# Performance work log

Measured on AMD Instinct MI355X. Metric: run time of the kernel, lower is better.

The kernel has to match this reference:

```python
import jax, jax.numpy as jnp
import numpy as np

SIZE = 2.0            # scene extent, matches init size
N_LEVELS = 16         # Instant-NGP default
TABLE_SIZE = 1 << 19  # hash entries per level (power of 2)
FEAT = 2              # embedding_length per level
BASE_RES = 16         # init resolution
MAX_RES = 2048
N_POINTS = 1 << 21

_OFFS = np.array([[(c >> d) & 1 for d in range(3)] for c in range(8)])  # [8,3] corner bits
_PRIMES = np.array([1, 2654435761, 805459861], dtype=np.uint32)         # NGP spatial hash primes


def setup_inputs() -> dict:
    key = jax.random.key(0)
    k1, k2 = jax.random.split(key)
    xyz = (jax.random.uniform(k1, (N_POINTS, 3), dtype=jnp.float32) - 0.5) * SIZE
    tables = jax.random.normal(k2, (N_LEVELS, TABLE_SIZE, FEAT), dtype=jnp.float32) * 1e-2
    # geometric resolution schedule 16 -> 2048 over 16 levels
    growth = (MAX_RES / BASE_RES) ** (np.arange(N_LEVELS) / (N_LEVELS - 1))
    resolutions = jnp.asarray(np.floor(BASE_RES * growth).astype(np.int32))
    return {"xyz": xyz, "tables": tables, "resolutions": resolutions}


def _encode(xyz, tables, resolutions):
    u = xyz / SIZE + 0.5                              # [N,3] in [0,1)
    offs_u = jnp.asarray(_OFFS.astype(np.uint32))     # [8,3]
    offs_f = jnp.asarray(_OFFS.astype(np.float32))    # [8,3]
    primes = jnp.asarray(_PRIMES)

    def level(_, xs):
        table, res = xs                               # [T,F], scalar int32
        p = u * res.astype(jnp.float32)               # [N,3]
        p0 = jnp.floor(p)
        w = p - p0                                    # trilinear fractions [N,3]
        c = p0.astype(jnp.uint32)[:, None, :] + offs_u[None]     # [N,8,3]
        h = (c[..., 0] * primes[0]) ^ (c[..., 1] * primes[1]) ^ (c[..., 2] * primes[2])
        idx = (h & jnp.uint32(TABLE_SIZE - 1)).astype(jnp.int32)  # [N,8]
        feats = table[idx]                                        # [N,8,F] gather
        wc = jnp.prod(jnp.where(offs_f[None] > 0, w[:, None, :], 1.0 - w[:, None, :]), axis=-1)  # [N,8]
        return None, jnp.sum(feats * wc[..., None], axis=1)      # [N,F]

    _, embs = jax.lax.scan(level, None, (tables, resolutions))   # [L,N,F]
    n = xyz.shape[0]
    return jnp.transpose(embs, (1, 0, 2)).reshape(n, N_LEVELS * FEAT)


def reference(xyz, tables, resolutions):
    return _encode(xyz, tables, resolutions)
```

## Files before the change

kernel.cpp:

```cpp
#include <hip/hip_runtime.h>
#include <hip/hip_fp16.h>

#define NLV 16
#define TBL (1u << 19)
#define TMASK (TBL - 1u)
#define P1 2654435761u
#define P2 805459861u
#define NBIN (1 << 15)

typedef float vf2 __attribute__((ext_vector_type(2)));
typedef float vf4 __attribute__((ext_vector_type(4)));
typedef unsigned vu2 __attribute__((ext_vector_type(2)));
typedef unsigned vu4 __attribute__((ext_vector_type(4)));
typedef int vi4 __attribute__((ext_vector_type(4)));

__device__ __forceinline__ vf2 h2_to_f2(unsigned bits) {
    union { unsigned u; __half2 h; } c; c.u = bits;
    float2 f = __half22float2(c.h);
    vf2 r; r.x = f.x; r.y = f.y; return r;
}
__device__ __forceinline__ unsigned f2_to_h2(float a, float b) {
    union { __half2 h; unsigned u; } c; c.h = __floats2half2_rn(a, b);
    return c.u;
}

__device__ __forceinline__ unsigned mort5(unsigned v) {
    v &= 31u;
    v = (v | (v << 16)) & 0x030000FFu;
    v = (v | (v << 8))  & 0x0300F00Fu;
    v = (v | (v << 4))  & 0x030C30C3u;
    v = (v | (v << 2))  & 0x09249249u;
    return v;
}

__device__ __forceinline__ unsigned bin_of(float ux, float uy, float uz) {
    unsigned bx = min(31u, (unsigned)(ux * 32.0f));
    unsigned by = min(31u, (unsigned)(uy * 32.0f));
    unsigned bz = min(31u, (unsigned)(uz * 32.0f));
    return mort5(bx) | (mort5(by) << 1) | (mort5(bz) << 2);
}

__global__ __launch_bounds__(256) void convert_tables(
    const float* __restrict__ tables, unsigned* __restrict__ htab, int total)
{
    int i = blockIdx.x * 256 + threadIdx.x;
    int e0 = i * 2;
    if (e0 >= total) return;
    vf4 v = *(const vf4*)(tables + (size_t)e0 * 2);
    vu2 o; o.x = f2_to_h2(v.x, v.y); o.y = f2_to_h2(v.z, v.w);
    *(vu2*)(htab + e0) = o;
}

__global__ __launch_bounds__(256) void hist_kernel(
    const float* __restrict__ xyz, unsigned* __restrict__ hist, int n)
{
    int p = blockIdx.x * 256 + threadIdx.x;
    if (p >= n) return;
    float ux = xyz[(size_t)p * 3 + 0] * 0.5f + 0.5f;
    float uy = xyz[(size_t)p * 3 + 1] * 0.5f + 0.5f;
    float uz = xyz[(size_t)p * 3 + 2] * 0.5f + 0.5f;
    atomicAdd(&hist[bin_of(ux, uy, uz)], 1u);
}

__global__ __launch_bounds__(1024) void scan_bins(unsigned* __restrict__ hist)
{
    __shared__ unsigned part[1024];
    int t = threadIdx.x;
    int base = t * (NBIN / 1024);
    unsigned s = 0;
    for (int j = 0; j < NBIN / 1024; ++j) s += hist[base + j];
    part[t] = s;
    __syncthreads();
    for (int off = 1; off < 1024; off <<= 1) {
        unsigned v = (t >= off) ? part[t - off] : 0u;
        __syncthreads();
        part[t] += v;
        __syncthreads();
    }
    unsigned run = (t == 0) ? 0u : part[t - 1];
    for (int j = 0; j < NBIN / 1024; ++j) {
        unsigned tmp = hist[base + j];
        hist[base + j] = run;
        run += tmp;
    }
}

__global__ __launch_bounds__(256) void scatter_kernel(
    const float* __restrict__ xyz, unsigned* __restrict__ start,
    vf4* __restrict__ u4s, int* __restrict__ orig, int n)
{
    int p = blockIdx.x * 256 + threadIdx.x;
    if (p >= n) return;
    float ux = xyz[(size_t)p * 3 + 0] * 0.5f + 0.5f;
    float uy = xyz[(size_t)p * 3 + 1] * 0.5f + 0.5f;
    float uz = xyz[(size_t)p * 3 + 2] * 0.5f + 0.5f;
    unsigned pos = atomicAdd(&start[bin_of(ux, uy, uz)], 1u);
    orig[pos] = p;
    vf4 r; r.x = ux; r.y = uy; r.z = uz; r.w = 0.0f;
    u4s[pos] = r;
}

__global__ __launch_bounds__(256) void ngp_gather_s(
    const vf4* __restrict__ u4s,
    const unsigned* __restrict__ htab,
    const int* __restrict__ resolutions,
    unsigned* __restrict__ wsout,
    int n, int nbPerLevel)
{
    int L = blockIdx.x / nbPerLevel;
    int chunk = blockIdx.x % nbPerLevel;
    int p0 = chunk * 1024 + (int)threadIdx.x;

    float res = (float)resolutions[L];
    const unsigned* __restrict__ tab = htab + (size_t)L * TBL;
    unsigned* __restrict__ wl = wsout + (size_t)L * n;

    unsigned idx[4][8];
    float wx[4], wyz[4][4];
    bool valid[4];

#pragma unroll
    for (int q = 0; q < 4; ++q) {
        int p = p0 + q * 256;
        valid[q] = (p < n);
        int pp = valid[q] ? p : 0;
        vf4 u = u4s[pp];
        float px = u.x * res, py = u.y * res, pz = u.z * res;
        float fx = floorf(px), fy = floorf(py), fz = floorf(pz);
        float wxl = px - fx, wyl = py - fy, wzl = pz - fz;
        unsigned cx = (unsigned)fx, cy = (unsigned)fy, cz = (unsigned)fz;
        unsigned hx0 = cx, hx1 = cx + 1u;
        unsigned hy0 = cy * P1, hy1 = hy0 + P1;
        unsigned hz0 = cz * P2, hz1 = hz0 + P2;
#pragma unroll
        for (int c = 0; c < 8; ++c)
            idx[q][c] = ((((c & 1) ? hx1 : hx0) ^
                          ((c & 2) ? hy1 : hy0) ^
                          ((c & 4) ? hz1 : hz0)) & TMASK);
        float vy = 1.0f - wyl, vz = 1.0f - wzl;
        wx[q] = wxl;
        wyz[q][0] = vy * vz;  wyz[q][1] = wyl * vz;
        wyz[q][2] = vy * wzl; wyz[q][3] = wyl * wzl;
    }

    unsigned d[4][8];
#pragma unroll
    for (int q = 0; q < 4; ++q)
#pragma unroll
        for (int c = 0; c < 8; ++c)
            d[q][c] = tab[idx[q][c]];

#pragma unroll
    for (int q = 0; q < 4; ++q) {
        float vx = 1.0f - wx[q];
        float a0 = 0.0f, a1 = 0.0f;
#pragma unroll
        for (int c = 0; c < 8; ++c) {
            float w = wyz[q][c >> 1] * ((c & 1) ? wx[q] : vx);
            vf2 f = h2_to_f2(d[q][c]);
            a0 += f.x * w;
            a1 += f.y * w;
        }
        int p = p0 + q * 256;
        if (valid[q]) wl[p] = f2_to_h2(a0, a1);
    }
}

__global__ __launch_bounds__(256) void ngp_finalize_s(
    const unsigned* __restrict__ ws, const int* __restrict__ orig,
    float* __restrict__ out, int n)
{
    int t = blockIdx.x * 256 + threadIdx.x;
    int i = t * 4;
    if (i >= n) return;

    if (i + 3 < n && (n & 3) == 0) {
        vu4 m[NLV];
#pragma unroll
        for (int L = 0; L < NLV; ++L)
            m[L] = *(const vu4*)(ws + (size_t)L * n + i);
        vi4 og = *(const vi4*)(orig + i);
#pragma unroll
        for (int pt = 0; pt < 4; ++pt) {
            int op = pt == 0 ? og.x : pt == 1 ? og.y : pt == 2 ? og.z : og.w;
            vf4* o = (vf4*)(out + (size_t)op * (NLV * 2));
#pragma unroll
            for (int j = 0; j < 8; ++j) {
                unsigned ba = pt == 0 ? m[2 * j].x : pt == 1 ? m[2 * j].y
                             : pt == 2 ? m[2 * j].z : m[2 * j].w;
                unsigned bb = pt == 0 ? m[2 * j + 1].x : pt == 1 ? m[2 * j + 1].y
                             : pt == 2 ? m[2 * j + 1].z : m[2 * j + 1].w;
                vf2 ga = h2_to_f2(ba), gb = h2_to_f2(bb);
                vf4 r; r.x = ga.x; r.y = ga.y; r.z = gb.x; r.w = gb.y;
                o[j] = r;
            }
        }
    } else {
        for (int pt = 0; pt < 4 && i + pt < n; ++pt) {
            int op = orig[i + pt];
            vf4* o = (vf4*)(out + (size_t)op * (NLV * 2));
#pragma unroll
            for (int j = 0; j < 8; ++j) {
                vf2 ga = h2_to_f2(ws[(size_t)(2 * j) * n + i + pt]);
                vf2 gb = h2_to_f2(ws[(size_t)(2 * j + 1) * n + i + pt]);
                vf4 r; r.x = ga.x; r.y = ga.y; r.z = gb.x; r.w = gb.y;
                o[j] = r;
            }
        }
    }
}

__global__ __launch_bounds__(256) void ngp_encode_kernel(
    const float* __restrict__ xyz,
    const float* __restrict__ tables,
    const int* __restrict__ resolutions,
    float* __restrict__ out,
    int n)
{
    int p = blockIdx.x * blockDim.x + threadIdx.x;
    if (p >= n) return;

    float x = xyz[(size_t)p * 3 + 0];
    float y = xyz[(size_t)p * 3 + 1];
    float z = xyz[(size_t)p * 3 + 2];
    float ux = x * 0.5f + 0.5f;
    float uy = y * 0.5f + 0.5f;
    float uz = z * 0.5f + 0.5f;

    float acc[NLV * 2];

#pragma unroll
    for (int L = 0; L < NLV; ++L) {
        float res = (float)resolutions[L];
        float px = ux * res, py = uy * res, pz = uz * res;
        float fx = floorf(px), fy = floorf(py), fz = floorf(pz);
        float wx = px - fx, wy = py - fy, wz = pz - fz;
        unsigned cx = (unsigned)fx, cy = (unsigned)fy, cz = (unsigned)fz;
        unsigned hx0 = cx, hx1 = cx + 1u;
        unsigned hy0 = cy * P1, hy1 = hy0 + P1;
        unsigned hz0 = cz * P2, hz1 = hz0 + P2;
        const vf2* __restrict__ tab = (const vf2*)tables + (size_t)L * TBL;
        float vx = 1.0f - wx, vy = 1.0f - wy, vz = 1.0f - wz;
        float a0 = 0.0f, a1 = 0.0f;
#pragma unroll
        for (int c = 0; c < 8; ++c) {
            unsigned h = ((c & 1) ? hx1 : hx0) ^
                         ((c & 2) ? hy1 : hy0) ^
                         ((c & 4) ? hz1 : hz0);
            vf2 f = tab[h & TMASK];
            float w = ((c & 1) ? wx : vx) *
                      ((c & 2) ? wy : vy) *
                      ((c & 4) ? wz : vz);
            a0 += f.x * w;
            a1 += f.y * w;
        }
        acc[L * 2 + 0] = a0;
        acc[L * 2 + 1] = a1;
    }

    vf4* o = (vf4*)(out + (size_t)p * (NLV * 2));
#pragma unroll
    for (int i = 0; i < 8; ++i) {
        vf4 r; r.x = acc[i * 4 + 0]; r.y = acc[i * 4 + 1];
        r.z = acc[i * 4 + 2]; r.w = acc[i * 4 + 3];
        o[i] = r;
    }
}

extern "C" void kernel_launch(void* const* d_in, const int* in_sizes, int n_in,
                              void* d_out, int out_size, void* d_ws, size_t ws_size,
                              hipStream_t stream) {
    const float* xyz = (const float*)d_in[0];
    const float* tables = (const float*)d_in[1];
    const int* resolutions = (const int*)d_in[2];
    float* out = (float*)d_out;

    int n = in_sizes[0] / 3;
    const int totalEntries = NLV * (int)TBL;

    const size_t tabBytes  = (size_t)totalEntries * 4;
    const size_t u4Bytes   = (size_t)n * sizeof(vf4);
    const size_t origBytes = (size_t)n * 4;
    const size_t histBytes = (size_t)NBIN * 4;
    const size_t wsoutBytes = (size_t)NLV * (size_t)n * 4;
    const size_t need = tabBytes + u4Bytes + origBytes + histBytes + wsoutBytes;

    if (ws_size >= need) {
        char* base = (char*)d_ws;
        unsigned* htab  = (unsigned*)base;                       base += tabBytes;
        vf4*      u4s   = (vf4*)base;                            base += u4Bytes;
        int*      orig  = (int*)base;                            base += origBytes;
        unsigned* hist  = (unsigned*)base;                       base += histBytes;
        unsigned* wsout = (unsigned*)base;

        hipMemsetAsync(hist, 0, histBytes, stream);

        int gridC = (totalEntries / 2 + 255) / 256;
        hipLaunchKernelGGL(convert_tables, dim3(gridC), dim3(256), 0, stream,
                           tables, htab, totalEntries);

        int gridP = (n + 255) / 256;
        hipLaunchKernelGGL(hist_kernel, dim3(gridP), dim3(256), 0, stream,
                           xyz, hist, n);
        hipLaunchKernelGGL(scan_bins, dim3(1), dim3(1024), 0, stream, hist);
        hipLaunchKernelGGL(scatter_kernel, dim3(gridP), dim3(256), 0, stream,
                           xyz, hist, u4s, orig, n);

        int nbPerLevel = (n + 1023) / 1024;
        int grid1 = NLV * nbPerLevel;
        hipLaunchKernelGGL(ngp_gather_s, dim3(grid1), dim3(256), 0, stream,
                           u4s, htab, resolutions, wsout, n, nbPerLevel);

        int gridF = ((n + 3) / 4 + 255) / 256;
        hipLaunchKernelGGL(ngp_finalize_s, dim3(gridF), dim3(256), 0, stream,
                           wsout, orig, out, n);
    } else {
        int grid = (n + 255) / 256;
        hipLaunchKernelGGL(ngp_encode_kernel, dim3(grid), dim3(256), 0, stream,
                           xyz, tables, resolutions, out, n);
    }
}
```

Before: 807.8 us.

## Fuse table conversion with histogram, vectorize xyz loads, split gather launch

Merges the fp16 table conversion and the spatial-bin histogram into a single launch, with blocks picking their role from the block index. The histogram and scatter kernels now handle four points per thread using vectorized 16-byte loads of xyz instead of scalar strided loads. The gather is split into two launches of eight levels each on the same stream. This removes one launch and cuts load instructions, at the cost of fewer threads in the point kernels and one extra gather launch.

```diff
diff --git a/kernel.cpp b/kernel.cpp
--- a/kernel.cpp
+++ b/kernel.cpp
@@ -40,26 +40,39 @@
     return mort5(bx) | (mort5(by) << 1) | (mort5(bz) << 2);
 }
 
-__global__ __launch_bounds__(256) void convert_tables(
-    const float* __restrict__ tables, unsigned* __restrict__ htab, int total)
-{
-    int i = blockIdx.x * 256 + threadIdx.x;
-    int e0 = i * 2;
-    if (e0 >= total) return;
-    vf4 v = *(const vf4*)(tables + (size_t)e0 * 2);
-    vu2 o; o.x = f2_to_h2(v.x, v.y); o.y = f2_to_h2(v.z, v.w);
-    *(vu2*)(htab + e0) = o;
-}
-
-__global__ __launch_bounds__(256) void hist_kernel(
-    const float* __restrict__ xyz, unsigned* __restrict__ hist, int n)
-{
-    int p = blockIdx.x * 256 + threadIdx.x;
-    if (p >= n) return;
-    float ux = xyz[(size_t)p * 3 + 0] * 0.5f + 0.5f;
-    float uy = xyz[(size_t)p * 3 + 1] * 0.5f + 0.5f;
-    float uz = xyz[(size_t)p * 3 + 2] * 0.5f + 0.5f;
-    atomicAdd(&hist[bin_of(ux, uy, uz)], 1u);
+__global__ __launch_bounds__(256) void convert_and_hist(
+    const float* __restrict__ tables, unsigned* __restrict__ htab, int total,
+    const float* __restrict__ xyz, unsigned* __restrict__ hist, int n,
+    int gridC)
+{
+    if ((int)blockIdx.x < gridC) {
+        int i = blockIdx.x * 256 + threadIdx.x;
+        int e0 = i * 2;
+        if (e0 >= total) return;
+        vf4 v = *(const vf4*)(tables + (size_t)e0 * 2);
+        vu2 o; o.x = f2_to_h2(v.x, v.y); o.y = f2_to_h2(v.z, v.w);
+        *(vu2*)(htab + e0) = o;
+    } else {
+        int t = (blockIdx.x - gridC) * 256 + threadIdx.x;
+        int p = t * 4;
+        if (p >= n) return;
+        if (p + 3 < n) {
+            vf4 a = *(const vf4*)(xyz + (size_t)p * 3);
+            vf4 b = *(const vf4*)(xyz + (size_t)p * 3 + 4);
+            vf4 c = *(const vf4*)(xyz + (size_t)p * 3 + 8);
+            atomicAdd(&hist[bin_of(a.x*0.5f+0.5f, a.y*0.5f+0.5f, a.z*0.5f+0.5f)], 1u);
+            atomicAdd(&hist[bin_of(a.w*0.5f+0.5f, b.x*0.5f+0.5f, b.y*0.5f+0.5f)], 1u);
+            atomicAdd(&hist[bin_of(b.z*0.5f+0.5f, b.w*0.5f+0.5f, c.x*0.5f+0.5f)], 1u);
+            atomicAdd(&hist[bin_of(c.y*0.5f+0.5f, c.z*0.5f+0.5f, c.w*0.5f+0.5f)], 1u);
+        } else {
+            for (int q = 0; q < 4 && p + q < n; ++q) {
+                float ux = xyz[(size_t)(p+q)*3+0]*0.5f+0.5f;
+                float uy = xyz[(size_t)(p+q)*3+1]*0.5f+0.5f;
+                float uz = xyz[(size_t)(p+q)*3+2]*0.5f+0.5f;
+                atomicAdd(&hist[bin_of(ux,uy,uz)], 1u);
+            }
+        }
+    }
 }
 
 __global__ __launch_bounds__(1024) void scan_bins(unsigned* __restrict__ hist)
@@ -89,15 +102,35 @@
     const float* __restrict__ xyz, unsigned* __restrict__ start,
     vf4* __restrict__ u4s, int* __restrict__ orig, int n)
 {
-    int p = blockIdx.x * 256 + threadIdx.x;
+    int t = blockIdx.x * 256 + threadIdx.x;
+    int p = t * 4;
     if (p >= n) return;
-    float ux = xyz[(size_t)p * 3 + 0] * 0.5f + 0.5f;
-    float uy = xyz[(size_t)p * 3 + 1] * 0.5f + 0.5f;
-    float uz = xyz[(size_t)p * 3 + 2] * 0.5f + 0.5f;
-    unsigned pos = atomicAdd(&start[bin_of(ux, uy, uz)], 1u);
-    orig[pos] = p;
-    vf4 r; r.x = ux; r.y = uy; r.z = uz; r.w = 0.0f;
-    u4s[pos] = r;
+    float U[4][3];
+    int cnt = (p + 3 < n) ? 4 : (n - p);
+    if (cnt == 4) {
+        vf4 a = *(const vf4*)(xyz + (size_t)p * 3);
+        vf4 b = *(const vf4*)(xyz + (size_t)p * 3 + 4);
+        vf4 c = *(const vf4*)(xyz + (size_t)p * 3 + 8);
+        U[0][0]=a.x; U[0][1]=a.y; U[0][2]=a.z;
+        U[1][0]=a.w; U[1][1]=b.x; U[1][2]=b.y;
+        U[2][0]=b.z; U[2][1]=b.w; U[2][2]=c.x;
+        U[3][0]=c.y; U[3][1]=c.z; U[3][2]=c.w;
+    } else {
+        for (int q = 0; q < cnt; ++q) {
+            U[q][0]=xyz[(size_t)(p+q)*3+0];
+            U[q][1]=xyz[(size_t)(p+q)*3+1];
+            U[q][2]=xyz[(size_t)(p+q)*3+2];
+        }
+    }
+#pragma unroll
+    for (int q = 0; q < 4; ++q) {
+        if (q >= cnt) break;
+        float ux = U[q][0]*0.5f+0.5f, uy = U[q][1]*0.5f+0.5f, uz = U[q][2]*0.5f+0.5f;
+        unsigned pos = atomicAdd(&start[bin_of(ux,uy,uz)], 1u);
+        orig[pos] = p + q;
+        vf4 r; r.x = ux; r.y = uy; r.z = uz; r.w = 0.0f;
+        u4s[pos] = r;
+    }
 }
 
 __global__ __launch_bounds__(256) void ngp_gather_s(
@@ -105,9 +138,9 @@
     const unsigned* __restrict__ htab,
     const int* __restrict__ resolutions,
     unsigned* __restrict__ wsout,
-    int n, int nbPerLevel)
-{
-    int L = blockIdx.x / nbPerLevel;
+    int n, int nbPerLevel, int Lbase)
+{
+    int L = Lbase + blockIdx.x / nbPerLevel;
     int chunk = blockIdx.x % nbPerLevel;
     int p0 = chunk * 1024 + (int)threadIdx.x;
 
@@ -296,20 +329,20 @@
         hipMemsetAsync(hist, 0, histBytes, stream);
 
         int gridC = (totalEntries / 2 + 255) / 256;
-        hipLaunchKernelGGL(convert_tables, dim3(gridC), dim3(256), 0, stream,
-                           tables, htab, totalEntries);
-
-        int gridP = (n + 255) / 256;
-        hipLaunchKernelGGL(hist_kernel, dim3(gridP), dim3(256), 0, stream,
-                           xyz, hist, n);
+        int grid4 = ((n + 3) / 4 + 255) / 256;
+        hipLaunchKernelGGL(convert_and_hist, dim3(gridC + grid4), dim3(256), 0,
+                           stream, tables, htab, totalEntries, xyz, hist, n, gridC);
+
         hipLaunchKernelGGL(scan_bins, dim3(1), dim3(1024), 0, stream, hist);
-        hipLaunchKernelGGL(scatter_kernel, dim3(gridP), dim3(256), 0, stream,
+        hipLaunchKernelGGL(scatter_kernel, dim3(grid4), dim3(256), 0, stream,
                            xyz, hist, u4s, orig, n);
 
         int nbPerLevel = (n + 1023) / 1024;
-        int grid1 = NLV * nbPerLevel;
-        hipLaunchKernelGGL(ngp_gather_s, dim3(grid1), dim3(256), 0, stream,
-                           u4s, htab, resolutions, wsout, n, nbPerLevel);
+        int gridHalf = 8 * nbPerLevel;
+        hipLaunchKernelGGL(ngp_gather_s, dim3(gridHalf), dim3(256), 0, stream,
+                           u4s, htab, resolutions, wsout, n, nbPerLevel, 0);
+        hipLaunchKernelGGL(ngp_gather_s, dim3(gridHalf), dim3(256), 0, stream,
+                           u4s, htab, resolutions, wsout, n, nbPerLevel, 8);
 
         int gridF = ((n + 3) / 4 + 255) / 256;
         hipLaunchKernelGGL(ngp_finalize_s, dim3(gridF), dim3(256), 0, stream,
```

After: 811.2 us. Within noise of the previous version (+0.4%).
